# Performance work log

Measured on AMD Instinct MI355X. Metric: run time of the kernel, lower is better.

## Reference

```python
import jax, jax.numpy as jnp
import numpy as np

H, W = 512, 512  # output_size from init_kwargs
N, C = 2_000_000, 64
EPS = 1e-6


def setup_inputs() -> dict:
    key = jax.random.key(0)
    k1, k2 = jax.random.split(key)
    features = jax.random.normal(k1, (N, C), dtype=jnp.float32)
    coordinates = jax.random.randint(k2, (N, 3), 0, 256, dtype=jnp.int32)
    # pinhole-like projection: u = (W/256)*x / (z+1), v = (H/256)*y / (z+1), depth = z+1 > 0
    projection_matrix = jnp.array(
        [[W / 256.0, 0.0, 0.0, 0.0],
         [0.0, H / 256.0, 0.0, 0.0],
         [0.0, 0.0, 1.0, 1.0]], dtype=jnp.float32)
    return {"features": features, "coordinates": coordinates,
            "projection_matrix": projection_matrix}


def reference(features, coordinates, projection_matrix):
    n = features.shape[0]
    coords_h = jnp.concatenate(
        [coordinates.astype(features.dtype),
         jnp.ones((n, 1), features.dtype)], axis=1)          # (N, 4)
    p = coords_h @ projection_matrix.T                        # (N, 3): (u*w, v*w, w)
    depth = p[:, 2]
    safe_d = jnp.where(depth > EPS, depth, 1.0)
    u = jnp.floor(p[:, 0] / safe_d).astype(jnp.int32)
    v = jnp.floor(p[:, 1] / safe_d).astype(jnp.int32)
    valid = (depth > EPS) & (u >= 0) & (u < W) & (v >= 0) & (v < H)
    flat = jnp.where(valid, v * W + u, 0)                     # dummy pixel 0 for invalid
    d = jnp.where(valid, depth, jnp.inf)
    # z-buffer: per-pixel min depth
    depth_buffer = jnp.full((H * W,), jnp.inf, features.dtype).at[flat].min(d)
    winner = valid & (d == depth_buffer[flat])
    idx_map = jnp.full((H * W,), -1, jnp.int32).at[flat].max(
        jnp.where(winner, jnp.arange(n, dtype=jnp.int32), -1))
    occupied = idx_map >= 0
    out_feats = jnp.where(occupied[:, None],
                          features[jnp.clip(idx_map, 0)],
                          jnp.zeros((), features.dtype)).reshape(H, W, -1)
    inv_depth_map = jnp.where(occupied, 1.0 / depth_buffer, 0.0).reshape(H, W)
    return out_feats, inv_depth_map
```

## Files before the change

### kernel.cpp

```cpp
#include <hip/hip_runtime.h>

#define WIDTH  512
#define HEIGHT 512
#define NPIX   (WIDTH * HEIGHT)
#define EPS_F  1e-6f

#define HOTW 32
#define HOTN (HOTW * HOTW)
#define PBLOCKS 256
#define PTHREADS 1024
#define RSPLIT 16

__device__ __forceinline__ unsigned long long u64min(unsigned long long a,
                                                     unsigned long long b) {
    return a < b ? a : b;
}

__device__ __forceinline__ void lds_min_filtered(unsigned long long* slot,
                                                 unsigned long long key) {
    unsigned long long cur = __atomic_load_n(slot, __ATOMIC_RELAXED);
    if (key < cur) atomicMin(slot, key);
}

__global__ __launch_bounds__(PTHREADS) void vp_points_slab(
        const int* __restrict__ coords,
        const float* __restrict__ proj,
        unsigned long long* __restrict__ packed,
        unsigned long long* __restrict__ slab,
        int n) {
    __shared__ unsigned long long lmin[HOTN];
    for (int s = threadIdx.x; s < HOTN; s += PTHREADS) lmin[s] = ~0ULL;
    __syncthreads();

    float p00 = proj[0], p01 = proj[1], p02 = proj[2],  p03 = proj[3];
    float p10 = proj[4], p11 = proj[5], p12 = proj[6],  p13 = proj[7];
    float p20 = proj[8], p21 = proj[9], p22 = proj[10], p23 = proj[11];

    int t0 = blockIdx.x * PTHREADS + threadIdx.x;
    int stride = gridDim.x * PTHREADS;
    int n4 = n >> 2;

    for (int i4 = t0; i4 < n4; i4 += stride) {
        const int4* cp = (const int4*)(coords + (size_t)i4 * 12);
        int4 a = cp[0], b = cp[1], c = cp[2];
        int xs[4] = {a.x, a.w, b.z, c.y};
        int ys[4] = {a.y, b.x, b.w, c.z};
        int zs[4] = {a.z, b.y, c.x, c.w};
#pragma unroll
        for (int r = 0; r < 4; ++r) {
            float x = (float)xs[r], y = (float)ys[r], z = (float)zs[r];
            float px = p00 * x + p01 * y + p02 * z + p03;
            float py = p10 * x + p11 * y + p12 * z + p13;
            float d  = p20 * x + p21 * y + p22 * z + p23;
            float sd = (d > EPS_F) ? d : 1.0f;
            int u = (int)floorf(px / sd);
            int v = (int)floorf(py / sd);
            if ((d > EPS_F) && (u >= 0) && (u < WIDTH) && (v >= 0) && (v < HEIGHT)) {
                int idx = i4 * 4 + r;
                unsigned long long key =
                    ((unsigned long long)__float_as_uint(d) << 32) |
                    (unsigned long long)(unsigned int)(~(unsigned int)idx);
                if ((unsigned)u < HOTW && (unsigned)v < HOTW) {
                    lds_min_filtered(&lmin[v * HOTW + u], key);
                } else {
                    atomicMin(&packed[v * WIDTH + u], key);
                }
            }
        }
    }
    int rem = n & 3;
    if (t0 < rem) {
        int i = n4 * 4 + t0;
        float x = (float)coords[i * 3 + 0];
        float y = (float)coords[i * 3 + 1];
        float z = (float)coords[i * 3 + 2];
        float px = p00 * x + p01 * y + p02 * z + p03;
        float py = p10 * x + p11 * y + p12 * z + p13;
        float d  = p20 * x + p21 * y + p22 * z + p23;
        float sd = (d > EPS_F) ? d : 1.0f;
        int u = (int)floorf(px / sd);
        int v = (int)floorf(py / sd);
        if ((d > EPS_F) && (u >= 0) && (u < WIDTH) && (v >= 0) && (v < HEIGHT)) {
            unsigned long long key =
                ((unsigned long long)__float_as_uint(d) << 32) |
                (unsigned long long)(unsigned int)(~(unsigned int)i);
            if ((unsigned)u < HOTW && (unsigned)v < HOTW)
                lds_min_filtered(&lmin[v * HOTW + u], key);
            else
                atomicMin(&packed[v * WIDTH + u], key);
        }
    }

    __syncthreads();
    unsigned long long* myslab = slab + (size_t)blockIdx.x * HOTN;
    for (int s = threadIdx.x; s < HOTN; s += PTHREADS) myslab[s] = lmin[s];
}

__global__ __launch_bounds__(256) void vp_reduce(
        const unsigned long long* __restrict__ slab,
        unsigned long long* __restrict__ packed) {
    int tid = blockIdx.x * 256 + threadIdx.x;
    int slot  = tid & (HOTN - 1);
    int chunk = tid / HOTN;
    const int per = PBLOCKS / RSPLIT;
    unsigned long long m = ~0ULL;
    const unsigned long long* p = slab + (size_t)chunk * per * HOTN + slot;
#pragma unroll 4
    for (int b = 0; b < per; ++b) m = u64min(m, p[(size_t)b * HOTN]);
    if (m != ~0ULL) {
        int pix = (slot / HOTW) * WIDTH + (slot & (HOTW - 1));
        atomicMin(&packed[pix], m);
    }
}

__global__ __launch_bounds__(256) void vp_gather(
        const unsigned long long* __restrict__ packed,
        const float* __restrict__ features,
        float* __restrict__ out_feats,
        float* __restrict__ inv_depth) {
    int tid = blockIdx.x * blockDim.x + threadIdx.x;
    int pix = tid >> 4;
    int c4  = tid & 15;
    if (pix >= NPIX) return;
    unsigned long long pk = packed[pix];
    float4 val = make_float4(0.f, 0.f, 0.f, 0.f);
    float invd = 0.f;
    if (pk != ~0ULL) {
        unsigned int idx = ~(unsigned int)(pk & 0xFFFFFFFFULL);
        float d = __uint_as_float((unsigned int)(pk >> 32));
        val = ((const float4*)features)[(size_t)idx * 16 + c4];
        invd = 1.0f / d;
    }
    __builtin_nontemporal_store(val.x, &out_feats[(size_t)pix * 64 + c4 * 4 + 0]);
    __builtin_nontemporal_store(val.y, &out_feats[(size_t)pix * 64 + c4 * 4 + 1]);
    __builtin_nontemporal_store(val.z, &out_feats[(size_t)pix * 64 + c4 * 4 + 2]);
    __builtin_nontemporal_store(val.w, &out_feats[(size_t)pix * 64 + c4 * 4 + 3]);
    if (c4 == 0) inv_depth[pix] = invd;
}

__global__ __launch_bounds__(256) void vp_points_atomic(
        const int* __restrict__ coords,
        const float* __restrict__ proj,
        unsigned long long* __restrict__ packed,
        int n) {
    __shared__ unsigned long long lmin[HOTN];
    for (int s = threadIdx.x; s < HOTN; s += 256) lmin[s] = ~0ULL;
    __syncthreads();
    float p00 = proj[0], p01 = proj[1], p02 = proj[2],  p03 = proj[3];
    float p10 = proj[4], p11 = proj[5], p12 = proj[6],  p13 = proj[7];
    float p20 = proj[8], p21 = proj[9], p22 = proj[10], p23 = proj[11];
    int i = blockIdx.x * blockDim.x + threadIdx.x;
    int stride = gridDim.x * blockDim.x;
    for (; i < n; i += stride) {
        float x = (float)coords[i * 3 + 0];
        float y = (float)coords[i * 3 + 1];
        float z = (float)coords[i * 3 + 2];
        float px = p00 * x + p01 * y + p02 * z + p03;
        float py = p10 * x + p11 * y + p12 * z + p13;
        float d  = p20 * x + p21 * y + p22 * z + p23;
        float sd = (d > EPS_F) ? d : 1.0f;
        int u = (int)floorf(px / sd);
        int v = (int)floorf(py / sd);
        if ((d > EPS_F) && (u >= 0) && (u < WIDTH) && (v >= 0) && (v < HEIGHT)) {
            unsigned long long key =
                ((unsigned long long)__float_as_uint(d) << 32) |
                (unsigned long long)(unsigned int)(~(unsigned int)i);
            if ((unsigned)u < HOTW && (unsigned)v < HOTW)
                lds_min_filtered(&lmin[v * HOTW + u], key);
            else
                atomicMin(&packed[v * WIDTH + u], key);
        }
    }
    __syncthreads();
    for (int s = threadIdx.x; s < HOTN; s += 256) {
        unsigned long long k = lmin[s];
        if (k != ~0ULL)
            atomicMin(&packed[(s / HOTW) * WIDTH + (s & (HOTW - 1))], k);
    }
}

extern "C" void kernel_launch(void* const* d_in, const int* in_sizes, int n_in,
                              void* d_out, int out_size, void* d_ws, size_t ws_size,
                              hipStream_t stream) {
    const float* features = (const float*)d_in[0];
    const int*   coords   = (const int*)d_in[1];
    const float* proj     = (const float*)d_in[2];
    int n = in_sizes[1] / 3;

    unsigned long long* packed = (unsigned long long*)d_ws;
    unsigned long long* slab   = packed + NPIX;

    float* out_feats = (float*)d_out;
    float* inv_depth = (float*)d_out + (size_t)NPIX * 64;

    (void)hipMemsetAsync(packed, 0xFF, (size_t)NPIX * 8, stream);

    size_t need = ((size_t)NPIX + (size_t)PBLOCKS * HOTN) * 8;
    if (ws_size >= need) {
        vp_points_slab<<<PBLOCKS, PTHREADS, 0, stream>>>(coords, proj, packed,
                                                         slab, n);
        vp_reduce<<<(HOTN * RSPLIT) / 256, 256, 0, stream>>>(slab, packed);
    } else {
        vp_points_atomic<<<512, 256, 0, stream>>>(coords, proj, packed, n);
    }

    vp_gather<<<(NPIX * 16 + 255) / 256, 256, 0, stream>>>(
        packed, features, out_feats, inv_depth);
}
```

Before: 37.09 us.

## Fuse hot-slab reduction into gather kernel and widen LDS hot region

The separate slab-reduce kernel is removed. Gather blocks that cover the hot corner now reduce the 256 per-block slab partials for their 16 pixels directly, using shared memory and 16-lane shuffles, instead of reading a pre-reduced packed buffer. The LDS-privatized hot region grows from 32x32 to 64x64 pixels, so more of the contended near-origin pixels avoid global 64-bit atomicMin. The trade-off is a 4x larger slab to write and read, 32KB of LDS per points block, and extra reduction work in the hot gather blocks. The fallback path keeps a separate simple gather.

```diff
diff --git a/kernel.cpp b/kernel.cpp
--- a/kernel.cpp
+++ b/kernel.cpp
@@ -5,11 +5,10 @@
 #define NPIX   (WIDTH * HEIGHT)
 #define EPS_F  1e-6f
 
-#define HOTW 32
+#define HOTW 64
 #define HOTN (HOTW * HOTW)
 #define PBLOCKS 256
 #define PTHREADS 1024
-#define RSPLIT 16
 
 __device__ __forceinline__ unsigned long long u64min(unsigned long long a,
                                                      unsigned long long b) {
@@ -96,33 +95,45 @@
     for (int s = threadIdx.x; s < HOTN; s += PTHREADS) myslab[s] = lmin[s];
 }
 
-__global__ __launch_bounds__(256) void vp_reduce(
-        const unsigned long long* __restrict__ slab,
-        unsigned long long* __restrict__ packed) {
-    int tid = blockIdx.x * 256 + threadIdx.x;
-    int slot  = tid & (HOTN - 1);
-    int chunk = tid / HOTN;
-    const int per = PBLOCKS / RSPLIT;
-    unsigned long long m = ~0ULL;
-    const unsigned long long* p = slab + (size_t)chunk * per * HOTN + slot;
-#pragma unroll 4
-    for (int b = 0; b < per; ++b) m = u64min(m, p[(size_t)b * HOTN]);
-    if (m != ~0ULL) {
-        int pix = (slot / HOTW) * WIDTH + (slot & (HOTW - 1));
-        atomicMin(&packed[pix], m);
-    }
-}
-
 __global__ __launch_bounds__(256) void vp_gather(
         const unsigned long long* __restrict__ packed,
+        const unsigned long long* __restrict__ slab,
         const float* __restrict__ features,
         float* __restrict__ out_feats,
         float* __restrict__ inv_depth) {
-    int tid = blockIdx.x * blockDim.x + threadIdx.x;
-    int pix = tid >> 4;
-    int c4  = tid & 15;
-    if (pix >= NPIX) return;
-    unsigned long long pk = packed[pix];
+    int b = blockIdx.x;
+    int t = threadIdx.x;
+    int pix0 = b * 16;
+    int pixl = t >> 4;
+    int c4   = t & 15;
+    int row  = pix0 >> 9;
+    int col0 = pix0 & 511;
+
+    bool hot_block = (row < HOTW) && (col0 < HOTW);
+    unsigned long long pk;
+
+    if (hot_block) {
+        __shared__ unsigned long long partial[16][17];
+        int slot_base = row * HOTW + col0;
+        int jg = t >> 4;
+        unsigned long long m = ~0ULL;
+        const unsigned long long* p = slab + slot_base + c4;
+#pragma unroll 4
+        for (int k = 0; k < 16; ++k) {
+            m = u64min(m, p[(size_t)(jg + 16 * k) * HOTN]);
+        }
+        partial[jg][c4] = m;
+        __syncthreads();
+        unsigned long long v = partial[c4][pixl];
+#pragma unroll
+        for (int mk = 8; mk >= 1; mk >>= 1)
+            v = u64min(v, (unsigned long long)__shfl_xor((long long)v, mk, 16));
+        pk = v;
+    } else {
+        pk = packed[pix0 + pixl];
+    }
+
+    int pix = pix0 + pixl;
     float4 val = make_float4(0.f, 0.f, 0.f, 0.f);
     float invd = 0.f;
     if (pk != ~0ULL) {
@@ -179,6 +190,28 @@
     }
 }
 
+__global__ __launch_bounds__(256) void vp_gather_simple(
+        const unsigned long long* __restrict__ packed,
+        const float* __restrict__ features,
+        float* __restrict__ out_feats,
+        float* __restrict__ inv_depth) {
+    int tid = blockIdx.x * blockDim.x + threadIdx.x;
+    int pix = tid >> 4;
+    int c4  = tid & 15;
+    if (pix >= NPIX) return;
+    unsigned long long pk = packed[pix];
+    float4 val = make_float4(0.f, 0.f, 0.f, 0.f);
+    float invd = 0.f;
+    if (pk != ~0ULL) {
+        unsigned int idx = ~(unsigned int)(pk & 0xFFFFFFFFULL);
+        float d = __uint_as_float((unsigned int)(pk >> 32));
+        val = ((const float4*)features)[(size_t)idx * 16 + c4];
+        invd = 1.0f / d;
+    }
+    ((float4*)out_feats)[(size_t)pix * 16 + c4] = val;
+    if (c4 == 0) inv_depth[pix] = invd;
+}
+
 extern "C" void kernel_launch(void* const* d_in, const int* in_sizes, int n_in,
                               void* d_out, int out_size, void* d_ws, size_t ws_size,
                               hipStream_t stream) {
@@ -199,11 +232,11 @@
     if (ws_size >= need) {
         vp_points_slab<<<PBLOCKS, PTHREADS, 0, stream>>>(coords, proj, packed,
                                                          slab, n);
-        vp_reduce<<<(HOTN * RSPLIT) / 256, 256, 0, stream>>>(slab, packed);
+        vp_gather<<<NPIX / 16, 256, 0, stream>>>(packed, slab, features,
+                                                 out_feats, inv_depth);
     } else {
         vp_points_atomic<<<512, 256, 0, stream>>>(coords, proj, packed, n);
-    }
-
-    vp_gather<<<(NPIX * 16 + 255) / 256, 256, 0, stream>>>(
-        packed, features, out_feats, inv_depth);
-}
+        vp_gather_simple<<<(NPIX * 16 + 255) / 256, 256, 0, stream>>>(
+            packed, features, out_feats, inv_depth);
+    }
+}
```

Measured after the change: 33.26 us. -10.3%, faster.
